# Performance work log

Hardware: AMD Instinct MI355X
Metric: run time of the kernel (lower is better)

## Reference

```python
import jax, jax.numpy as jnp
import numpy as np

D_MODEL = 1024
D_STATE = 32
D_CONV = 4
D_INNER = 2 * D_MODEL          # mamba default expand=2
DT_RANK = D_MODEL // 16        # 'auto' -> ceil(d_model/16)
BATCH, SEQ = 4, 2048
LN_EPS = 1e-5


def setup_inputs() -> dict:
    key = jax.random.key(0)
    ks = jax.random.split(key, 8)
    s = 0.02
    # S4D-real init for A_log, as in mamba_ssm
    A_log = jnp.log(jnp.tile(jnp.arange(1, D_STATE + 1, dtype=jnp.float32)[None, :], (D_INNER, 1)))
    return {
        "x": jax.random.normal(ks[0], (BATCH, SEQ, D_MODEL), jnp.float32),
        "in_proj_w": jax.random.normal(ks[1], (D_MODEL, 2 * D_INNER), jnp.float32) * s,
        "conv_w": jax.random.normal(ks[2], (D_INNER, D_CONV), jnp.float32) * s,
        "conv_b": jnp.zeros((D_INNER,), jnp.float32),
        "x_proj_w": jax.random.normal(ks[3], (D_INNER, DT_RANK + 2 * D_STATE), jnp.float32) * s,
        "dt_proj_w": jax.random.normal(ks[4], (DT_RANK, D_INNER), jnp.float32) * s,
        "dt_proj_b": jax.random.uniform(ks[5], (D_INNER,), jnp.float32, -4.0, -2.0),  # softplus -> small dt
        "A_log": A_log,
        "D": jnp.ones((D_INNER,), jnp.float32),
        "out_proj_w": jax.random.normal(ks[6], (D_INNER, D_MODEL), jnp.float32) * s,
        "ln_gamma": jnp.ones((D_MODEL,), jnp.float32),
        "ln_beta": jnp.zeros((D_MODEL,), jnp.float32),
    }


def reference(x, in_proj_w, conv_w, conv_b, x_proj_w, dt_proj_w, dt_proj_b,
              A_log, D, out_proj_w, ln_gamma, ln_beta):
    Bb, Ll, _ = x.shape
    # in_proj -> split into ssm branch (xi) and gate (z)
    xz = x @ in_proj_w                              # [B,L,2*Di]
    xi, z = jnp.split(xz, 2, axis=-1)               # each [B,L,Di]

    # causal depthwise conv1d (kernel D_CONV), left-padded, truncated to L
    xp = jnp.pad(xi, ((0, 0), (D_CONV - 1, 0), (0, 0)))
    xc = conv_b
    for k in range(D_CONV):
        xc = xc + xp[:, k:k + Ll, :] * conv_w[None, None, :, k]
    xi = jax.nn.silu(xc)                            # [B,L,Di]

    # x_proj -> dt, B, C
    dbc = xi @ x_proj_w                             # [B,L,dt_rank+2*S]
    dt = dbc[..., :DT_RANK]
    Bm = dbc[..., DT_RANK:DT_RANK + D_STATE]        # [B,L,S]
    Cm = dbc[..., DT_RANK + D_STATE:]               # [B,L,S]
    delta = jax.nn.softplus(dt @ dt_proj_w + dt_proj_b)  # [B,L,Di]

    A = -jnp.exp(A_log)                             # [Di,S]

    def step(h, inp):
        dl, bt, ct, ut = inp                        # [B,Di],[B,S],[B,S],[B,Di]
        dA = jnp.exp(dl[..., None] * A)             # [B,Di,S]
        h = dA * h + (dl * ut)[..., None] * bt[:, None, :]
        y = jnp.einsum('bds,bs->bd', h, ct)
        return h, y

    h0 = jnp.zeros((Bb, D_INNER, D_STATE), x.dtype)
    xs = (delta.transpose(1, 0, 2), Bm.transpose(1, 0, 2),
          Cm.transpose(1, 0, 2), xi.transpose(1, 0, 2))
    _, ys = jax.lax.scan(step, h0, xs)              # ys: [L,B,Di]

    y = ys.transpose(1, 0, 2) + xi * D              # skip term u*D
    y = y * jax.nn.silu(z)                          # gate
    out = y @ out_proj_w                            # [B,L,d_model]

    # LayerNorm(d_model)
    mu = out.mean(-1, keepdims=True)
    var = out.var(-1, keepdims=True)
    return (out - mu) / jnp.sqrt(var + LN_EPS) * ln_gamma + ln_beta
```

## Files before the change

### kernel.cpp

```cpp
#include <hip/hip_runtime.h>
#include <math.h>

#define D_MODEL 1024
#define D_STATE 32
#define D_CONV  4
#define D_INNER 2048
#define DT_RANK 64
#define BATCH   4
#define SEQ     2048
#define NTOK    (BATCH*SEQ)
#define DBC_N   (DT_RANK + 2*D_STATE)
#define NC      32
#define CL      (SEQ/NC)
#define KSPLIT  4
#define LOG2E   1.4426950408889634f

typedef unsigned short u16;
typedef short bf16x8 __attribute__((ext_vector_type(8)));
typedef float f32x4  __attribute__((ext_vector_type(4)));
typedef u16   u16x8  __attribute__((ext_vector_type(8)));

__device__ __forceinline__ float bf2f(u16 u){
  return __uint_as_float(((unsigned)u) << 16);
}
__device__ __forceinline__ u16 f2bf(float f){
  unsigned u = __float_as_uint(f);
  return (u16)((u + 0x7fffu + ((u >> 16) & 1u)) >> 16);
}
__device__ __forceinline__ float sigmoidf_(float x){ return 1.f/(1.f+__expf(-x)); }
__device__ __forceinline__ float exp2_fast(float x){
  float r;
  asm("v_exp_f32 %0, %1" : "=v"(r) : "v"(x));
  return r;
}

typedef __attribute__((address_space(3))) void       lds_v;
typedef const __attribute__((address_space(1))) void gl_v;
#define GLOAD_LDS16(g, l) \
  __builtin_amdgcn_global_load_lds((gl_v*)(g), (lds_v*)(l), 16, 0, 0)

template<int MODE>
__global__ __launch_bounds__(256)
void mfma_gemm(int K,
               const u16* __restrict__ A, int lda,
               const u16* __restrict__ B, int ldb,
               void* __restrict__ C1, int ldc,
               u16*  __restrict__ C2,
               const float* __restrict__ bias)
{
  __shared__ u16 As[128*64];
  __shared__ u16 Bs[128*64];
  const int tid  = threadIdx.x;
  const int lane = tid & 63;
  const int wave = tid >> 6;
  const int wm = (wave>>1)*64, wn = (wave&1)*64;
  const int m0 = blockIdx.y*128, n0 = blockIdx.x*128;
  const size_t koff = (MODE==3) ? (size_t)blockIdx.z*K : 0;

  const int srow = tid >> 3;
  const int sch  = ((tid & 7) ^ (srow & 7)) * 8;

  const u16* Ag = A + (size_t)(m0 + srow)*lda + sch + koff;
  const u16* Bg = B + (size_t)(n0 + srow)*ldb + sch + koff;

  const int fr = lane & 15;
  const int fq = lane >> 4;
  const int rkey = (fr & 7);
  f32x4 acc[4][4] = {};

  for (int k0=0; k0<K; k0+=64){
    #pragma unroll
    for (int g=0; g<4; ++g){
      GLOAD_LDS16(Ag + (size_t)(32*g)*lda + k0, &As[g*2048 + tid*8]);
      GLOAD_LDS16(Bg + (size_t)(32*g)*ldb + k0, &Bs[g*2048 + tid*8]);
    }
    __syncthreads();

    #pragma unroll
    for (int ks=0; ks<2; ++ks){
      const int rc = ((ks*4 + fq) ^ rkey) * 8;
      bf16x8 af[4], bfr[4];
      #pragma unroll
      for (int i=0;i<4;i++){
        af[i]  = *(const bf16x8*)&As[(wm + i*16 + fr)*64 + rc];
        bfr[i] = *(const bf16x8*)&Bs[(wn + i*16 + fr)*64 + rc];
      }
      #pragma unroll
      for (int mi=0;mi<4;mi++)
        #pragma unroll
        for (int ni=0;ni<4;ni++)
          acc[mi][ni] = __builtin_amdgcn_mfma_f32_16x16x32_bf16(
              af[mi], bfr[ni], acc[mi][ni], 0, 0, 0);
    }
    __syncthreads();
  }

  float* Cf = (float*)C1;
  if (MODE==3) Cf += (size_t)blockIdx.z*((size_t)NTOK*DBC_N);

  const bool second = (MODE==2) && (n0 >= D_INNER);
  #pragma unroll
  for (int mi=0;mi<4;mi++){
    #pragma unroll
    for (int ni=0;ni<4;ni++){
      int col = n0 + wn + ni*16 + fr;
      #pragma unroll
      for (int r=0;r<4;r++){
        int row = m0 + wm + mi*16 + fq*4 + r;
        float v = acc[mi][ni][r];
        if (MODE==0 || MODE==3){
          Cf[(size_t)row*ldc + col] = v;
        } else if (MODE==4){
          v += bias[col];
          v = (v > 20.f) ? v : log1pf(__expf(v));
          ((u16*)C1)[(size_t)row*ldc + col] = f2bf(v);
        } else {
          if (second) C2[(size_t)row*D_INNER + (col - D_INNER)] = f2bf(v);
          else        ((u16*)C1)[(size_t)row*D_INNER + col]     = f2bf(v);
        }
      }
    }
  }
}

__global__ __launch_bounds__(256)
void cvt_f32_bf16(const float* __restrict__ in, u16* __restrict__ out)
{
  size_t i = (size_t)blockIdx.x*256 + threadIdx.x;
  float4 v = ((const float4*)in)[i];
  ushort4 o;
  o.x=f2bf(v.x); o.y=f2bf(v.y); o.z=f2bf(v.z); o.w=f2bf(v.w);
  ((ushort4*)out)[i] = o;
}

__global__ __launch_bounds__(256)
void transpose_cvt(const float* __restrict__ in, u16* __restrict__ out,
                   int R, int C)
{
  __shared__ float tile[64][65];
  const int bc = blockIdx.x*64, br = blockIdx.y*64;
  const int tx = threadIdx.x & 63, ty = threadIdx.x >> 6;
  #pragma unroll
  for (int i=0;i<16;i++){
    int r = ty + i*4;
    tile[r][tx] = in[(size_t)(br+r)*C + bc+tx];
  }
  __syncthreads();
  #pragma unroll
  for (int i=0;i<16;i++){
    int r = ty + i*4;
    out[(size_t)(bc+r)*R + br+tx] = f2bf(tile[tx][r]);
  }
}

__global__ __launch_bounds__(256)
void reduce_pk(const float* __restrict__ part, float* __restrict__ dbc,
               u16* __restrict__ dtbf)
{
  size_t i = (size_t)blockIdx.x*256 + threadIdx.x;
  const size_t stride4 = (size_t)NTOK*DBC_N/4;
  float4 s = ((const float4*)part)[i];
  #pragma unroll
  for (int z=1; z<KSPLIT; ++z){
    float4 v = ((const float4*)part)[z*stride4 + i];
    s.x+=v.x; s.y+=v.y; s.z+=v.z; s.w+=v.w;
  }
  ((float4*)dbc)[i] = s;
  int j = (int)(i & 31);
  if (j < 16){
    size_t row = i >> 5;
    ushort4 o;
    o.x=f2bf(s.x); o.y=f2bf(s.y); o.z=f2bf(s.z); o.w=f2bf(s.w);
    *(ushort4*)(dtbf + row*DT_RANK + 4*j) = o;
  }
}

__global__ __launch_bounds__(256)
void conv_silu_kernel(const u16* __restrict__ xi_bf,
                      const float* __restrict__ conv_w,
                      const float* __restrict__ conv_b,
                      u16* __restrict__ u_bf)
{
  size_t i8 = (size_t)blockIdx.x*256 + threadIdx.x;
  size_t base = i8*8;
  int d0 = (int)(base % D_INNER);
  size_t bt = base / D_INNER;
  int t = (int)(bt % SEQ);
  size_t b = bt / SEQ;
  const u16* xi = xi_bf + b*(size_t)SEQ*D_INNER + d0;

  float accv[8];
  #pragma unroll
  for (int j=0;j<8;j++) accv[j] = conv_b[d0+j];
  float4 cw[8];
  #pragma unroll
  for (int j=0;j<8;j++) cw[j] = *(const float4*)(conv_w + (size_t)(d0+j)*D_CONV);

  #pragma unroll
  for (int k=0;k<D_CONV;k++){
    int tt = t + k - (D_CONV-1);
    if (tt >= 0){
      u16x8 v = *(const u16x8*)(xi + (size_t)tt*D_INNER);
      const float* w = (const float*)&cw[0];
      accv[0] += bf2f(v[0]) * ((const float*)&cw[0])[k];
      accv[1] += bf2f(v[1]) * ((const float*)&cw[1])[k];
      accv[2] += bf2f(v[2]) * ((const float*)&cw[2])[k];
      accv[3] += bf2f(v[3]) * ((const float*)&cw[3])[k];
      accv[4] += bf2f(v[4]) * ((const float*)&cw[4])[k];
      accv[5] += bf2f(v[5]) * ((const float*)&cw[5])[k];
      accv[6] += bf2f(v[6]) * ((const float*)&cw[6])[k];
      accv[7] += bf2f(v[7]) * ((const float*)&cw[7])[k];
      (void)w;
    }
  }
  u16x8 o;
  #pragma unroll
  for (int j=0;j<8;j++){
    float r = accv[j] * sigmoidf_(accv[j]);
    o[j] = f2bf(r);
  }
  *(u16x8*)(u_bf + base) = o;
}

__global__ __launch_bounds__(256)
void scan_part1(const float* __restrict__ dbc,
                const u16*   __restrict__ delta,
                const u16*   __restrict__ u,
                const float* __restrict__ A_log,
                float* __restrict__ q,
                float* __restrict__ sumdl_buf)
{
  const int ndg  = D_INNER/256;
  const int dgrp = blockIdx.x % ndg;
  const int c    = (blockIdx.x / ndg) % NC;
  const int b    =  blockIdx.x / (ndg*NC);
  const int d    = dgrp*256 + threadIdx.x;

  const float* Ap = A_log + (size_t)d*D_STATE;
  const float base = -__expf(Ap[0]) * LOG2E;
  bool fastp = true;
  #pragma unroll
  for (int s=1; s<D_STATE; ++s){
    float a2 = -__expf(Ap[s]) * LOG2E;
    float ideal = base * (float)(s+1);
    fastp = fastp && (fabsf(a2 - ideal) <= 1e-4f*fabsf(ideal));
  }

  const size_t tok0 = (size_t)b*SEQ + (size_t)c*CL;
  const u16*   dptr = delta + tok0*D_INNER + d;
  const u16*   uptr = u     + tok0*D_INNER + d;
  const float* dbcp = dbc   + tok0*DBC_N;

  float h[D_STATE] = {};
  float sumdl = 0.f;

  if (fastp){
    for (int t=0; t<CL; ++t){
      float dl = bf2f(dptr[(size_t)t*D_INNER]);
      float uu = bf2f(uptr[(size_t)t*D_INNER]);
      sumdl += dl;
      float w  = dl*uu;
      float E  = exp2_fast(dl*base);
      float E2 = E*E, E3 = E2*E, E4 = E2*E2;
      float P  = 1.f;
      const float4* B4 = (const float4*)(dbcp + (size_t)t*DBC_N + DT_RANK);
      #pragma unroll
      for (int g=0; g<8; ++g){
        float4 Bv = B4[g];
        float m0 = P*E, m1 = P*E2, m2 = P*E3, m3 = P*E4;
        h[4*g+0] = m0*h[4*g+0] + w*Bv.x;
        h[4*g+1] = m1*h[4*g+1] + w*Bv.y;
        h[4*g+2] = m2*h[4*g+2] + w*Bv.z;
        h[4*g+3] = m3*h[4*g+3] + w*Bv.w;
        P = m3;
      }
    }
  } else {
    float A2[D_STATE];
    #pragma unroll
    for (int g=0; g<8; ++g){
      float4 al = *(const float4*)(Ap + 4*g);
      A2[4*g+0] = -__expf(al.x)*LOG2E; A2[4*g+1] = -__expf(al.y)*LOG2E;
      A2[4*g+2] = -__expf(al.z)*LOG2E; A2[4*g+3] = -__expf(al.w)*LOG2E;
    }
    for (int t=0; t<CL; ++t){
      float dl = bf2f(dptr[(size_t)t*D_INNER]);
      float uu = bf2f(uptr[(size_t)t*D_INNER]);
      sumdl += dl;
      float w = dl*uu;
      const float4* B4 = (const float4*)(dbcp + (size_t)t*DBC_N + DT_RANK);
      #pragma unroll
      for (int g=0; g<8; ++g){
        float4 Bv = B4[g];
        h[4*g+0] = exp2_fast(dl*A2[4*g+0])*h[4*g+0] + w*Bv.x;
        h[4*g+1] = exp2_fast(dl*A2[4*g+1])*h[4*g+1] + w*Bv.y;
        h[4*g+2] = exp2_fast(dl*A2[4*g+2])*h[4*g+2] + w*Bv.z;
        h[4*g+3] = exp2_fast(dl*A2[4*g+3])*h[4*g+3] + w*Bv.w;
      }
    }
  }

  float* qp = q + (((size_t)b*NC + c)*D_INNER + d)*D_STATE;
  #pragma unroll
  for (int g=0; g<8; ++g)
    ((float4*)qp)[g] = make_float4(h[4*g+0],h[4*g+1],h[4*g+2],h[4*g+3]);
  sumdl_buf[((size_t)b*NC + c)*D_INNER + d] = sumdl;
}

__global__ __launch_bounds__(256)
void scan_combine(float* __restrict__ q,
                  const float* __restrict__ sumdl_buf,
                  const float* __restrict__ A_log)
{
  size_t idx = (size_t)blockIdx.x*256 + threadIdx.x;
  int s = (int)(idx % D_STATE);
  size_t dd = idx / D_STATE;
  int d = (int)(dd % D_INNER);
  int b = (int)(dd / D_INNER);

  const float As2 = -__expf(A_log[(size_t)d*D_STATE + s]) * LOG2E;
  float H = 0.f;
  for (int c=0; c<NC; ++c){
    size_t off = (((size_t)b*NC + c)*D_INNER + d)*D_STATE + s;
    float tmp = q[off];
    q[off] = H;
    H = exp2_fast(As2 * sumdl_buf[((size_t)b*NC + c)*D_INNER + d]) * H + tmp;
  }
}

__global__ __launch_bounds__(256)
void scan_part2(const float* __restrict__ dbc,
                const u16*   __restrict__ delta,
                const u16*   __restrict__ u,
                u16*         __restrict__ zy,
                const float* __restrict__ q,
                const float* __restrict__ A_log,
                const float* __restrict__ Dp)
{
  const int ndg  = D_INNER/256;
  const int dgrp = blockIdx.x % ndg;
  const int c    = (blockIdx.x / ndg) % NC;
  const int b    =  blockIdx.x / (ndg*NC);
  const int d    = dgrp*256 + threadIdx.x;

  const float* Ap = A_log + (size_t)d*D_STATE;
  const float base = -__expf(Ap[0]) * LOG2E;
  bool fastp = true;
  #pragma unroll
  for (int s=1; s<D_STATE; ++s){
    float a2 = -__expf(Ap[s]) * LOG2E;
    float ideal = base * (float)(s+1);
    fastp = fastp && (fabsf(a2 - ideal) <= 1e-4f*fabsf(ideal));
  }

  float h[D_STATE];
  const float* qp = q + (((size_t)b*NC + c)*D_INNER + d)*D_STATE;
  #pragma unroll
  for (int g=0; g<8; ++g){
    float4 hv = ((const float4*)qp)[g];
    h[4*g+0]=hv.x; h[4*g+1]=hv.y; h[4*g+2]=hv.z; h[4*g+3]=hv.w;
  }
  const float Dd = Dp[d];

  const size_t tok0 = (size_t)b*SEQ + (size_t)c*CL;
  const u16*   dptr = delta + tok0*D_INNER + d;
  const u16*   uptr = u     + tok0*D_INNER + d;
  u16*         zp   = zy    + tok0*D_INNER + d;
  const float* dbcp = dbc   + tok0*DBC_N;

  if (fastp){
    for (int t=0; t<CL; ++t){
      float dl = bf2f(dptr[(size_t)t*D_INNER]);
      float uu = bf2f(uptr[(size_t)t*D_INNER]);
      float zz = bf2f(zp[(size_t)t*D_INNER]);
      float w  = dl*uu;
      float E  = exp2_fast(dl*base);
      float E2 = E*E, E3 = E2*E, E4 = E2*E2;
      float P  = 1.f;
      const float4* B4 = (const float4*)(dbcp + (size_t)t*DBC_N + DT_RANK);
      const float4* C4 = B4 + 8;
      float y = 0.f;
      #pragma unroll
      for (int g=0; g<8; ++g){
        float4 Bv = B4[g];
        float4 Cv = C4[g];
        float m0 = P*E, m1 = P*E2, m2 = P*E3, m3 = P*E4;
        h[4*g+0] = m0*h[4*g+0] + w*Bv.x;  y += h[4*g+0]*Cv.x;
        h[4*g+1] = m1*h[4*g+1] + w*Bv.y;  y += h[4*g+1]*Cv.y;
        h[4*g+2] = m2*h[4*g+2] + w*Bv.z;  y += h[4*g+2]*Cv.z;
        h[4*g+3] = m3*h[4*g+3] + w*Bv.w;  y += h[4*g+3]*Cv.w;
        P = m3;
      }
      zp[(size_t)t*D_INNER] = f2bf((y + uu*Dd) * (zz * sigmoidf_(zz)));
    }
  } else {
    float A2[D_STATE];
    #pragma unroll
    for (int g=0; g<8; ++g){
      float4 al = *(const float4*)(Ap + 4*g);
      A2[4*g+0] = -__expf(al.x)*LOG2E; A2[4*g+1] = -__expf(al.y)*LOG2E;
      A2[4*g+2] = -__expf(al.z)*LOG2E; A2[4*g+3] = -__expf(al.w)*LOG2E;
    }
    for (int t=0; t<CL; ++t){
      float dl = bf2f(dptr[(size_t)t*D_INNER]);
      float uu = bf2f(uptr[(size_t)t*D_INNER]);
      float zz = bf2f(zp[(size_t)t*D_INNER]);
      float w  = dl*uu;
      const float4* B4 = (const float4*)(dbcp + (size_t)t*DBC_N + DT_RANK);
      const float4* C4 = B4 + 8;
      float y = 0.f;
      #pragma unroll
      for (int g=0; g<8; ++g){
        float4 Bv = B4[g];
        float4 Cv = C4[g];
        h[4*g+0] = exp2_fast(dl*A2[4*g+0])*h[4*g+0] + w*Bv.x;  y += h[4*g+0]*Cv.x;
        h[4*g+1] = exp2_fast(dl*A2[4*g+1])*h[4*g+1] + w*Bv.y;  y += h[4*g+1]*Cv.y;
        h[4*g+2] = exp2_fast(dl*A2[4*g+2])*h[4*g+2] + w*Bv.z;  y += h[4*g+2]*Cv.z;
        h[4*g+3] = exp2_fast(dl*A2[4*g+3])*h[4*g+3] + w*Bv.w;  y += h[4*g+3]*Cv.w;
      }
      zp[(size_t)t*D_INNER] = f2bf((y + uu*Dd) * (zz * sigmoidf_(zz)));
    }
  }
}

__global__ __launch_bounds__(256)
void ln_kernel(const float* __restrict__ in,
               float* __restrict__ out,
               const float* __restrict__ gamma,
               const float* __restrict__ beta)
{
  const int row = blockIdx.x;
  const float* p = in + (size_t)row*D_MODEL;
  float* q = out + (size_t)row*D_MODEL;
  float4 v = ((const float4*)p)[threadIdx.x];
  float s  = v.x+v.y+v.z+v.w;
  float ss = v.x*v.x+v.y*v.y+v.z*v.z+v.w*v.w;
  #pragma unroll
  for (int off=32; off; off>>=1){
    s  += __shfl_xor(s,  off, 64);
    ss += __shfl_xor(ss, off, 64);
  }
  __shared__ float sw[4], ssw[4];
  const int wid = threadIdx.x >> 6;
  if ((threadIdx.x & 63) == 0){ sw[wid]=s; ssw[wid]=ss; }
  __syncthreads();
  s  = sw[0]+sw[1]+sw[2]+sw[3];
  ss = ssw[0]+ssw[1]+ssw[2]+ssw[3];
  const float mu  = s * (1.f/D_MODEL);
  const float var = ss * (1.f/D_MODEL) - mu*mu;
  const float inv = rsqrtf(var + 1e-5f);
  float4 gm = ((const float4*)gamma)[threadIdx.x];
  float4 bt = ((const float4*)beta )[threadIdx.x];
  float4 o;
  o.x = (v.x-mu)*inv*gm.x + bt.x;
  o.y = (v.y-mu)*inv*gm.y + bt.y;
  o.z = (v.z-mu)*inv*gm.z + bt.z;
  o.w = (v.w-mu)*inv*gm.w + bt.w;
  ((float4*)q)[threadIdx.x] = o;
}

extern "C" void kernel_launch(void* const* d_in, const int* in_sizes, int n_in,
                              void* d_out, int out_size, void* d_ws, size_t ws_size,
                              hipStream_t stream)
{
  const float* x          = (const float*)d_in[0];
  const float* in_proj_w  = (const float*)d_in[1];
  const float* conv_w     = (const float*)d_in[2];
  const float* conv_b     = (const float*)d_in[3];
  const float* x_proj_w   = (const float*)d_in[4];
  const float* dt_proj_w  = (const float*)d_in[5];
  const float* dt_proj_b  = (const float*)d_in[6];
  const float* A_log      = (const float*)d_in[7];
  const float* Dp         = (const float*)d_in[8];
  const float* out_proj_w = (const float*)d_in[9];
  const float* ln_gamma   = (const float*)d_in[10];
  const float* ln_beta    = (const float*)d_in[11];
  float* out = (float*)d_out;

  char* ws = (char*)d_ws;
  u16*   x_bf    = (u16*)  (ws + 0);
  float* pkpart  = (float*)(ws + 0);
  u16*   xi_bf   = (u16*)  (ws + (size_t) 33554432);
  float* qbuf    = (float*)(ws + (size_t) 33554432);
  u16*   u_bf    = (u16*)  (ws + (size_t) 67108864);
  u16*   zybuf   = (u16*)  (ws + (size_t)100663296);
  u16*   delta_bf= (u16*)  (ws + (size_t)134217728);
  float* dbc     = (float*)(ws + (size_t)167772160);
  u16*   dtbf    = (u16*)  (ws + (size_t)171966464);
  float* sumdl   = (float*)(ws + (size_t)173015040);
  float* preln   = (float*)(ws + (size_t)174063616);
  u16*   w_inT   = (u16*)  (ws + (size_t)207618048);
  u16*   w_outT  = (u16*)  (ws + (size_t)216006656);
  u16*   x_projT = (u16*)  (ws + (size_t)220200960);
  u16*   dt_projT= (u16*)  (ws + (size_t)220725248);

  cvt_f32_bf16<<<(NTOK*(size_t)D_MODEL)/1024, 256, 0, stream>>>(x, x_bf);
  { dim3 g(4096/64, 1024/64); transpose_cvt<<<g,256,0,stream>>>(in_proj_w,  w_inT,  1024, 4096); }
  { dim3 g(1024/64, 2048/64); transpose_cvt<<<g,256,0,stream>>>(out_proj_w, w_outT, 2048, 1024); }
  { dim3 g( 128/64, 2048/64); transpose_cvt<<<g,256,0,stream>>>(x_proj_w,   x_projT, 2048, 128); }
  { dim3 g(2048/64,   64/64); transpose_cvt<<<g,256,0,stream>>>(dt_proj_w,  dt_projT,  64, 2048); }

  {
    dim3 grid(2*D_INNER/128, NTOK/128);
    mfma_gemm<2><<<grid,256,0,stream>>>(D_MODEL,
        x_bf, D_MODEL, w_inT, D_MODEL, xi_bf, 0, zybuf, nullptr);
  }
  conv_silu_kernel<<<(NTOK*(size_t)D_INNER)/2048,256,0,stream>>>(
      xi_bf, conv_w, conv_b, u_bf);

  {
    dim3 grid(DBC_N/128, NTOK/128, KSPLIT);
    mfma_gemm<3><<<grid,256,0,stream>>>(D_INNER/KSPLIT,
        u_bf, D_INNER, x_projT, D_INNER, pkpart, DBC_N, nullptr, nullptr);
    reduce_pk<<<(NTOK*(size_t)DBC_N)/1024,256,0,stream>>>(pkpart, dbc, dtbf);
  }
  {
    dim3 grid(D_INNER/128, NTOK/128);
    mfma_gemm<4><<<grid,256,0,stream>>>(DT_RANK,
        dtbf, DT_RANK, dt_projT, DT_RANK, delta_bf, D_INNER, nullptr, dt_proj_b);
  }
  {
    dim3 grid1((D_INNER/256)*NC*BATCH);
    scan_part1<<<grid1,256,0,stream>>>(dbc, delta_bf, u_bf, A_log, qbuf, sumdl);
    scan_combine<<<(BATCH*(size_t)D_INNER*D_STATE)/256,256,0,stream>>>(qbuf, sumdl, A_log);
    scan_part2<<<grid1,256,0,stream>>>(dbc, delta_bf, u_bf, zybuf, qbuf, A_log, Dp);
  }
  {
    dim3 grid(D_MODEL/128, NTOK/128);
    mfma_gemm<0><<<grid,256,0,stream>>>(D_INNER,
        zybuf, D_INNER, w_outT, D_INNER, preln, D_MODEL, nullptr, nullptr);
  }
  ln_kernel<<<NTOK,256,0,stream>>>(preln, out, ln_gamma, ln_beta);
}
```

Measured before the change: 562.2 us.

## Split SSM state dimension across half-waves in chunked scan kernels

```diff
diff --git a/kernel.cpp b/kernel.cpp
--- a/kernel.cpp
+++ b/kernel.cpp
@@ -201,7 +201,6 @@
     int tt = t + k - (D_CONV-1);
     if (tt >= 0){
       u16x8 v = *(const u16x8*)(xi + (size_t)tt*D_INNER);
-      const float* w = (const float*)&cw[0];
       accv[0] += bf2f(v[0]) * ((const float*)&cw[0])[k];
       accv[1] += bf2f(v[1]) * ((const float*)&cw[1])[k];
       accv[2] += bf2f(v[2]) * ((const float*)&cw[2])[k];
@@ -210,7 +209,6 @@
       accv[5] += bf2f(v[5]) * ((const float*)&cw[5])[k];
       accv[6] += bf2f(v[6]) * ((const float*)&cw[6])[k];
       accv[7] += bf2f(v[7]) * ((const float*)&cw[7])[k];
-      (void)w;
     }
   }
   u16x8 o;
@@ -230,19 +228,23 @@
                 float* __restrict__ q,
                 float* __restrict__ sumdl_buf)
 {
-  const int ndg  = D_INNER/256;
+  const int ndg  = D_INNER/128;
   const int dgrp = blockIdx.x % ndg;
   const int c    = (blockIdx.x / ndg) % NC;
   const int b    =  blockIdx.x / (ndg*NC);
-  const int d    = dgrp*256 + threadIdx.x;
+  const int lane = threadIdx.x & 63;
+  const int wave = threadIdx.x >> 6;
+  const int half = lane >> 5;
+  const int d    = dgrp*128 + wave*32 + (lane & 31);
 
   const float* Ap = A_log + (size_t)d*D_STATE;
   const float base = -__expf(Ap[0]) * LOG2E;
   bool fastp = true;
   #pragma unroll
-  for (int s=1; s<D_STATE; ++s){
-    float a2 = -__expf(Ap[s]) * LOG2E;
-    float ideal = base * (float)(s+1);
+  for (int s=0; s<16; ++s){
+    int j = half*16 + s;
+    float a2 = -__expf(Ap[j]) * LOG2E;
+    float ideal = base * (float)(j+1);
     fastp = fastp && (fabsf(a2 - ideal) <= 1e-4f*fabsf(ideal));
   }
 
@@ -251,7 +253,7 @@
   const u16*   uptr = u     + tok0*D_INNER + d;
   const float* dbcp = dbc   + tok0*DBC_N;
 
-  float h[D_STATE] = {};
+  float h[16] = {};
   float sumdl = 0.f;
 
   if (fastp){
@@ -262,10 +264,12 @@
       float w  = dl*uu;
       float E  = exp2_fast(dl*base);
       float E2 = E*E, E3 = E2*E, E4 = E2*E2;
-      float P  = 1.f;
-      const float4* B4 = (const float4*)(dbcp + (size_t)t*DBC_N + DT_RANK);
-      #pragma unroll
-      for (int g=0; g<8; ++g){
+      float E8 = E4*E4;
+      float P  = half ? E8*E8 : 1.f;
+      const float4* B4 = (const float4*)(dbcp + (size_t)t*DBC_N + DT_RANK)
+                         + half*4;
+      #pragma unroll
+      for (int g=0; g<4; ++g){
         float4 Bv = B4[g];
         float m0 = P*E, m1 = P*E2, m2 = P*E3, m3 = P*E4;
         h[4*g+0] = m0*h[4*g+0] + w*Bv.x;
@@ -276,10 +280,10 @@
       }
     }
   } else {
-    float A2[D_STATE];
+    float A2[16];
     #pragma unroll
-    for (int g=0; g<8; ++g){
-      float4 al = *(const float4*)(Ap + 4*g);
+    for (int g=0; g<4; ++g){
+      float4 al = *(const float4*)(Ap + half*16 + 4*g);
       A2[4*g+0] = -__expf(al.x)*LOG2E; A2[4*g+1] = -__expf(al.y)*LOG2E;
       A2[4*g+2] = -__expf(al.z)*LOG2E; A2[4*g+3] = -__expf(al.w)*LOG2E;
     }
@@ -288,9 +292,10 @@
       float uu = bf2f(uptr[(size_t)t*D_INNER]);
       sumdl += dl;
       float w = dl*uu;
-      const float4* B4 = (const float4*)(dbcp + (size_t)t*DBC_N + DT_RANK);
-      #pragma unroll
-      for (int g=0; g<8; ++g){
+      const float4* B4 = (const float4*)(dbcp + (size_t)t*DBC_N + DT_RANK)
+                         + half*4;
+      #pragma unroll
+      for (int g=0; g<4; ++g){
         float4 Bv = B4[g];
         h[4*g+0] = exp2_fast(dl*A2[4*g+0])*h[4*g+0] + w*Bv.x;
         h[4*g+1] = exp2_fast(dl*A2[4*g+1])*h[4*g+1] + w*Bv.y;
@@ -300,11 +305,12 @@
     }
   }
 
-  float* qp = q + (((size_t)b*NC + c)*D_INNER + d)*D_STATE;
-  #pragma unroll
-  for (int g=0; g<8; ++g)
+  float* qp = q + (((size_t)b*NC + c)*D_INNER + d)*D_STATE + half*16;
+  #pragma unroll
+  for (int g=0; g<4; ++g)
     ((float4*)qp)[g] = make_float4(h[4*g+0],h[4*g+1],h[4*g+2],h[4*g+3]);
-  sumdl_buf[((size_t)b*NC + c)*D_INNER + d] = sumdl;
+  if (half == 0)
+    sumdl_buf[((size_t)b*NC + c)*D_INNER + d] = sumdl;
 }
 
 __global__ __launch_bounds__(256)
@@ -337,26 +343,30 @@
                 const float* __restrict__ A_log,
                 const float* __restrict__ Dp)
 {
-  const int ndg  = D_INNER/256;
+  const int ndg  = D_INNER/128;
   const int dgrp = blockIdx.x % ndg;
   const int c    = (blockIdx.x / ndg) % NC;
   const int b    =  blockIdx.x / (ndg*NC);
-  const int d    = dgrp*256 + threadIdx.x;
+  const int lane = threadIdx.x & 63;
+  const int wave = threadIdx.x >> 6;
+  const int half = lane >> 5;
+  const int d    = dgrp*128 + wave*32 + (lane & 31);
 
   const float* Ap = A_log + (size_t)d*D_STATE;
   const float base = -__expf(Ap[0]) * LOG2E;
   bool fastp = true;
   #pragma unroll
-  for (int s=1; s<D_STATE; ++s){
-    float a2 = -__expf(Ap[s]) * LOG2E;
-    float ideal = base * (float)(s+1);
+  for (int s=0; s<16; ++s){
+    int j = half*16 + s;
+    float a2 = -__expf(Ap[j]) * LOG2E;
+    float ideal = base * (float)(j+1);
     fastp = fastp && (fabsf(a2 - ideal) <= 1e-4f*fabsf(ideal));
   }
 
-  float h[D_STATE];
-  const float* qp = q + (((size_t)b*NC + c)*D_INNER + d)*D_STATE;
-  #pragma unroll
-  for (int g=0; g<8; ++g){
+  float h[16];
+  const float* qp = q + (((size_t)b*NC + c)*D_INNER + d)*D_STATE + half*16;
+  #pragma unroll
+  for (int g=0; g<4; ++g){
     float4 hv = ((const float4*)qp)[g];
     h[4*g+0]=hv.x; h[4*g+1]=hv.y; h[4*g+2]=hv.z; h[4*g+3]=hv.w;
   }
@@ -372,16 +382,17 @@
     for (int t=0; t<CL; ++t){
       float dl = bf2f(dptr[(size_t)t*D_INNER]);
       float uu = bf2f(uptr[(size_t)t*D_INNER]);
-      float zz = bf2f(zp[(size_t)t*D_INNER]);
       float w  = dl*uu;
       float E  = exp2_fast(dl*base);
       float E2 = E*E, E3 = E2*E, E4 = E2*E2;
-      float P  = 1.f;
-      const float4* B4 = (const float4*)(dbcp + (size_t)t*DBC_N + DT_RANK);
+      float E8 = E4*E4;
+      float P  = half ? E8*E8 : 1.f;
+      const float4* B4 = (const float4*)(dbcp + (size_t)t*DBC_N + DT_RANK)
+                         + half*4;
       const float4* C4 = B4 + 8;
       float y = 0.f;
       #pragma unroll
-      for (int g=0; g<8; ++g){
+      for (int g=0; g<4; ++g){
         float4 Bv = B4[g];
         float4 Cv = C4[g];
         float m0 = P*E, m1 = P*E2, m2 = P*E3, m3 = P*E4;
@@ -391,26 +402,30 @@
         h[4*g+3] = m3*h[4*g+3] + w*Bv.w;  y += h[4*g+3]*Cv.w;
         P = m3;
       }
-      zp[(size_t)t*D_INNER] = f2bf((y + uu*Dd) * (zz * sigmoidf_(zz)));
+      y += __shfl_xor(y, 32, 64);
+      if (half == 0){
+        float zz = bf2f(zp[(size_t)t*D_INNER]);
+        zp[(size_t)t*D_INNER] = f2bf((y + uu*Dd) * (zz * sigmoidf_(zz)));
+      }
     }
   } else {
-    float A2[D_STATE];
+    float A2[16];
     #pragma unroll
-    for (int g=0; g<8; ++g){
-      float4 al = *(const float4*)(Ap + 4*g);
+    for (int g=0; g<4; ++g){
+      float4 al = *(const float4*)(Ap + half*16 + 4*g);
       A2[4*g+0] = -__expf(al.x)*LOG2E; A2[4*g+1] = -__expf(al.y)*LOG2E;
       A2[4*g+2] = -__expf(al.z)*LOG2E; A2[4*g+3] = -__expf(al.w)*LOG2E;
     }
     for (int t=0; t<CL; ++t){
       float dl = bf2f(dptr[(size_t)t*D_INNER]);
       float uu = bf2f(uptr[(size_t)t*D_INNER]);
-      float zz = bf2f(zp[(size_t)t*D_INNER]);
       float w  = dl*uu;
-      const float4* B4 = (const float4*)(dbcp + (size_t)t*DBC_N + DT_RANK);
+      const float4* B4 = (const float4*)(dbcp + (size_t)t*DBC_N + DT_RANK)
+                         + half*4;
       const float4* C4 = B4 + 8;
       float y = 0.f;
       #pragma unroll
-      for (int g=0; g<8; ++g){
+      for (int g=0; g<4; ++g){
         float4 Bv = B4[g];
         float4 Cv = C4[g];
         h[4*g+0] = exp2_fast(dl*A2[4*g+0])*h[4*g+0] + w*Bv.x;  y += h[4*g+0]*Cv.x;
@@ -418,7 +433,11 @@
         h[4*g+2] = exp2_fast(dl*A2[4*g+2])*h[4*g+2] + w*Bv.z;  y += h[4*g+2]*Cv.z;
         h[4*g+3] = exp2_fast(dl*A2[4*g+3])*h[4*g+3] + w*Bv.w;  y += h[4*g+3]*Cv.w;
       }
-      zp[(size_t)t*D_INNER] = f2bf((y + uu*Dd) * (zz * sigmoidf_(zz)));
+      y += __shfl_xor(y, 32, 64);
+      if (half == 0){
+        float zz = bf2f(zp[(size_t)t*D_INNER]);
+        zp[(size_t)t*D_INNER] = f2bf((y + uu*Dd) * (zz * sigmoidf_(zz)));
+      }
     }
   }
 }
@@ -520,7 +539,7 @@
         dtbf, DT_RANK, dt_projT, DT_RANK, delta_bf, D_INNER, nullptr, dt_proj_b);
   }
   {
-    dim3 grid1((D_INNER/256)*NC*BATCH);
+    dim3 grid1((D_INNER/128)*NC*BATCH);
     scan_part1<<<grid1,256,0,stream>>>(dbc, delta_bf, u_bf, A_log, qbuf, sumdl);
     scan_combine<<<(BATCH*(size_t)D_INNER*D_STATE)/256,256,0,stream>>>(qbuf, sumdl, A_log);
     scan_part2<<<grid1,256,0,stream>>>(dbc, delta_bf, u_bf, zybuf, qbuf, A_log, Dp);
```

Result: slower. 691.5 us (+23.0%).
